# Optimization experiments

Hardware: AMD Instinct MI355X
Metric: run time of the kernel (lower is better)

Reference implementation:

```python
import math
import jax, jax.numpy as jnp
import numpy as np

CAPACITY = 2097152  # 2**21, power of two -> complete sum tree
SIZE = 1048576


def _build_tree(probs):
    # Tree layout: node i has children 2i+1, 2i+2; leaves are tree[-capacity:].
    # For power-of-two capacity this is levels concatenated root-first.
    levels = [probs]
    x = probs
    while x.shape[0] > 1:
        x = x.reshape(-1, 2).sum(axis=1)
        levels.append(x)
    return jnp.concatenate(levels[::-1])


def setup_inputs() -> dict:
    key = jax.random.key(0)
    k1, k2 = jax.random.split(key)
    priorities = jax.random.uniform(k1, (CAPACITY,), dtype=jnp.float32)
    uniform = jax.random.uniform(k2, (SIZE,), dtype=jnp.float32)
    return {"priorities": priorities, "uniform": uniform, "size": SIZE}


def reference(priorities, uniform, size):
    cap = priorities.shape[0]
    depth = int(math.log2(cap))  # number of traversal steps (complete tree)
    tree = _build_tree(priorities)  # [2*cap - 1]
    total = tree[0]

    # sample() with equal_mode=True: stratified samples in [0, total)
    offsets = jnp.linspace(0.0, total, size + 1, dtype=jnp.float32)[:-1]
    sums = uniform * total / size + offsets  # [size]
    idx0 = jnp.zeros((size,), dtype=jnp.int32)

    def body(_, carry):
        idx, s = carry
        left = 2 * idx + 1
        left_val = tree[left]            # gather [size]
        go_left = s <= left_val
        idx = jnp.where(go_left, left, left + 1)
        s = jnp.where(go_left, s, s - left_val)
        return idx, s

    idx, _ = jax.lax.fori_loop(0, depth, body, (idx0, sums))
    return idx - cap + 1  # leaf index in [0, cap)
```

## Files before the change

kernel.cpp:

```cpp
#include <hip/hip_runtime.h>


#define CAP    (1 << 21)
#define NSAMP  (1 << 20)
#define L18OFF ((1 << 18) - 1)

__global__ __launch_bounds__(256) void build_tree(const float* __restrict__ prio,
                                                  float* __restrict__ tree) {
    __shared__ __align__(16) float A[512];
    __shared__ __align__(16) float B[256];
    const int b = blockIdx.x, t = threadIdx.x;
    const float4* p4 = (const float4*)(prio + (size_t)b * 4096);

    #pragma unroll
    for (int i = t; i < 512; i += 256) {
        float4 x = p4[2 * i], y = p4[2 * i + 1];
        A[i] = ((x.x + x.y) + (x.z + x.w)) + ((y.x + y.y) + (y.z + y.w));
    }
    __syncthreads();
    {
        float* g = tree + L18OFF + b * 512;
        #pragma unroll
        for (int i = t; i < 512; i += 256) g[i] = A[i];
    }
    float* src = A;
    float* dst = B;
    int cnt = 256;
    int off = (1 << 17) - 1;
    for (int lvl = 17; lvl >= 9; --lvl) {
        for (int i = t; i < cnt; i += 256) {
            float2 v = ((const float2*)src)[i];
            float r = v.x + v.y;
            dst[i] = r;
            tree[off + b * cnt + i] = r;
        }
        __syncthreads();
        float* tmp = src; src = dst; dst = tmp;
        off = (off - 1) >> 1;
        cnt >>= 1;
    }
}

__global__ __launch_bounds__(256) void sample_kernel(const float* __restrict__ tree,
                                                     const float* __restrict__ prio,
                                                     const float* __restrict__ uniform,
                                                     int* __restrict__ out) {
    __shared__ float nds[8191];
    const int t = threadIdx.x;

    for (int i = 511 + t; i < 8191; i += 256) nds[i] = tree[i];
    __syncthreads();
    {
        int cnt = 256, off = 255;
        for (int lvl = 8; lvl >= 0; --lvl) {
            for (int i = t; i < cnt; i += 256) {
                int n = off + i;
                nds[n] = nds[2 * n + 1] + nds[2 * n + 2];
            }
            __syncthreads();
            off = (off - 1) >> 1;
            cnt >>= 1;
        }
    }

    const float total = nds[0];
    const float scale = total / (float)NSAMP;
    const int base = blockIdx.x * 1024 + t;

    float s[4];
    int   id[4];
    #pragma unroll
    for (int q = 0; q < 4; ++q) {
        int j = base + 256 * q;
        s[q]  = uniform[j] * total / (float)NSAMP + scale * (float)j;
        id[q] = 0;
    }

    #pragma unroll
    for (int d = 0; d < 12; ++d) {
        #pragma unroll
        for (int q = 0; q < 4; ++q) {
            int left = 2 * id[q] + 1;
            float lv = nds[left];
            bool r = s[q] > lv;
            s[q]  = r ? s[q] - lv : s[q];
            id[q] = r ? left + 1 : left;
        }
    }
    #pragma unroll
    for (int d = 0; d < 6; ++d) {
        #pragma unroll
        for (int q = 0; q < 4; ++q) {
            int left = 2 * id[q] + 1;
            float lv = tree[left];
            bool r = s[q] > lv;
            s[q]  = r ? s[q] - lv : s[q];
            id[q] = r ? left + 1 : left;
        }
    }
    #pragma unroll
    for (int q = 0; q < 4; ++q) {
        int p = id[q] - L18OFF;
        const float4* pp = (const float4*)prio + 2 * (size_t)p;
        float4 x = pp[0], y = pp[1];
        float l19 = (x.x + x.y) + (x.z + x.w);
        bool r1 = s[q] > l19;
        float ss = r1 ? s[q] - l19 : s[q];
        float l20 = r1 ? (y.x + y.y) : (x.x + x.y);
        bool r2 = ss > l20;
        ss = r2 ? ss - l20 : ss;
        float leaf = r1 ? (r2 ? y.z : y.x) : (r2 ? x.z : x.x);
        bool r3 = ss > leaf;
        out[base + 256 * q] = 8 * p + (r1 ? 4 : 0) + (r2 ? 2 : 0) + (r3 ? 1 : 0);
    }
}

extern "C" void kernel_launch(void* const* d_in, const int* in_sizes, int n_in,
                              void* d_out, int out_size, void* d_ws, size_t ws_size,
                              hipStream_t stream) {
    const float* prio    = (const float*)d_in[0];
    const float* uniform = (const float*)d_in[1];
    (void)in_sizes; (void)n_in; (void)out_size; (void)ws_size;

    float* tree = (float*)d_ws;

    build_tree<<<512, 256, 0, stream>>>(prio, tree);
    sample_kernel<<<NSAMP / 1024, 256, 0, stream>>>(tree, prio, uniform, (int*)d_out);
}
```

Baseline: 76.26 us.

## Fuse tree build and sampling into one kernel with a grid-wide atomic barrier

```diff
diff --git a/kernel.cpp b/kernel.cpp
--- a/kernel.cpp
+++ b/kernel.cpp
@@ -4,55 +4,54 @@
 #define CAP    (1 << 21)
 #define NSAMP  (1 << 20)
 #define L18OFF ((1 << 18) - 1)
+#define NBLK   1024
 
-__global__ __launch_bounds__(256) void build_tree(const float* __restrict__ prio,
-                                                  float* __restrict__ tree) {
-    __shared__ __align__(16) float A[512];
-    __shared__ __align__(16) float B[256];
+__global__ __launch_bounds__(256) void fused_kernel(const float* __restrict__ prio,
+                                                    const float* __restrict__ uniform,
+                                                    float* __restrict__ tree,
+                                                    unsigned int* __restrict__ bar,
+                                                    int* __restrict__ out) {
+    __shared__ __align__(16) float nds[8191];
     const int b = blockIdx.x, t = threadIdx.x;
-    const float4* p4 = (const float4*)(prio + (size_t)b * 4096);
 
-    #pragma unroll
-    for (int i = t; i < 512; i += 256) {
-        float4 x = p4[2 * i], y = p4[2 * i + 1];
-        A[i] = ((x.x + x.y) + (x.z + x.w)) + ((y.x + y.y) + (y.z + y.w));
+    {
+        const float4* p4 = (const float4*)(prio + (size_t)b * 2048);
+        float4 x = p4[2 * t], y = p4[2 * t + 1];
+        float n18 = ((x.x + x.y) + (x.z + x.w)) + ((y.x + y.y) + (y.z + y.w));
+        tree[L18OFF + b * 256 + t] = n18;
+        nds[t] = n18;
+        __syncthreads();
+        float* src = nds;
+        float* dst = nds + 4096;
+        int cnt = 128, off = (1 << 17) - 1;
+        for (int lvl = 17; lvl >= 10; --lvl) {
+            if (t < cnt) {
+                float r = src[2 * t] + src[2 * t + 1];
+                dst[t] = r;
+                tree[off + b * cnt + t] = r;
+            }
+            __syncthreads();
+            float* tmp = src; src = dst; dst = tmp;
+            off = (off - 1) >> 1;
+            cnt >>= 1;
+        }
+    }
+
+    __threadfence();
+    if (t == 0) {
+        __hip_atomic_fetch_add(bar, 1u, __ATOMIC_ACQ_REL, __HIP_MEMORY_SCOPE_AGENT);
+        while (__hip_atomic_load(bar, __ATOMIC_ACQUIRE, __HIP_MEMORY_SCOPE_AGENT) < NBLK) {
+            __builtin_amdgcn_s_sleep(8);
+        }
     }
     __syncthreads();
-    {
-        float* g = tree + L18OFF + b * 512;
-        #pragma unroll
-        for (int i = t; i < 512; i += 256) g[i] = A[i];
-    }
-    float* src = A;
-    float* dst = B;
-    int cnt = 256;
-    int off = (1 << 17) - 1;
-    for (int lvl = 17; lvl >= 9; --lvl) {
-        for (int i = t; i < cnt; i += 256) {
-            float2 v = ((const float2*)src)[i];
-            float r = v.x + v.y;
-            dst[i] = r;
-            tree[off + b * cnt + i] = r;
-        }
-        __syncthreads();
-        float* tmp = src; src = dst; dst = tmp;
-        off = (off - 1) >> 1;
-        cnt >>= 1;
-    }
-}
+    __threadfence();
 
-__global__ __launch_bounds__(256) void sample_kernel(const float* __restrict__ tree,
-                                                     const float* __restrict__ prio,
-                                                     const float* __restrict__ uniform,
-                                                     int* __restrict__ out) {
-    __shared__ float nds[8191];
-    const int t = threadIdx.x;
-
-    for (int i = 511 + t; i < 8191; i += 256) nds[i] = tree[i];
+    for (int i = 1023 + t; i < 8191; i += 256) nds[i] = tree[i];
     __syncthreads();
     {
-        int cnt = 256, off = 255;
-        for (int lvl = 8; lvl >= 0; --lvl) {
+        int cnt = 512, off = 511;
+        for (int lvl = 9; lvl >= 0; --lvl) {
             for (int i = t; i < cnt; i += 256) {
                 int n = off + i;
                 nds[n] = nds[2 * n + 1] + nds[2 * n + 2];
@@ -65,7 +64,7 @@
 
     const float total = nds[0];
     const float scale = total / (float)NSAMP;
-    const int base = blockIdx.x * 1024 + t;
+    const int base = b * 1024 + t;
 
     float s[4];
     int   id[4];
@@ -75,7 +74,6 @@
         s[q]  = uniform[j] * total / (float)NSAMP + scale * (float)j;
         id[q] = 0;
     }
-
     #pragma unroll
     for (int d = 0; d < 12; ++d) {
         #pragma unroll
@@ -123,7 +121,8 @@
     (void)in_sizes; (void)n_in; (void)out_size; (void)ws_size;
 
     float* tree = (float*)d_ws;
+    unsigned int* bar = (unsigned int*)((float*)d_ws + (1 << 20));
 
-    build_tree<<<512, 256, 0, stream>>>(prio, tree);
-    sample_kernel<<<NSAMP / 1024, 256, 0, stream>>>(tree, prio, uniform, (int*)d_out);
+    hipMemsetAsync(bar, 0, 4, stream);
+    fused_kernel<<<NBLK, 256, 0, stream>>>(prio, uniform, tree, bar, (int*)d_out);
 }
```

Measured after the change: 235.0 us. +208.1%, slower.

## Store lower tree levels as per-subtree contiguous blocks for cache-local traversal

Applied to the files above, without the earlier changes.

```diff
diff --git a/kernel.cpp b/kernel.cpp
--- a/kernel.cpp
+++ b/kernel.cpp
@@ -3,59 +3,66 @@
 
 #define CAP    (1 << 21)
 #define NSAMP  (1 << 20)
-#define L18OFF ((1 << 18) - 1)
 
 __global__ __launch_bounds__(256) void build_tree(const float* __restrict__ prio,
-                                                  float* __restrict__ tree) {
-    __shared__ __align__(16) float A[512];
-    __shared__ __align__(16) float B[256];
+                                                  float* __restrict__ tree,
+                                                  float* __restrict__ blocked) {
+    __shared__ float L18[512], L17[256], L16[128], L15[64], L14[32],
+                     L13[16],  L12[8],   L11[4],   L10[2];
+    __shared__ __align__(16) float rec[1024];
     const int b = blockIdx.x, t = threadIdx.x;
-    const float4* p4 = (const float4*)(prio + (size_t)b * 4096);
 
-    #pragma unroll
-    for (int i = t; i < 512; i += 256) {
-        float4 x = p4[2 * i], y = p4[2 * i + 1];
-        A[i] = ((x.x + x.y) + (x.z + x.w)) + ((y.x + y.y) + (y.z + y.w));
+    {
+        const float4* p4 = (const float4*)(prio + (size_t)b * 4096);
+        float4 x0 = p4[4*t+0], x1 = p4[4*t+1], x2 = p4[4*t+2], x3 = p4[4*t+3];
+        L18[2*t]   = ((x0.x+x0.y)+(x0.z+x0.w)) + ((x1.x+x1.y)+(x1.z+x1.w));
+        L18[2*t+1] = ((x2.x+x2.y)+(x2.z+x2.w)) + ((x3.x+x3.y)+(x3.z+x3.w));
     }
     __syncthreads();
-    {
-        float* g = tree + L18OFF + b * 512;
-        #pragma unroll
-        for (int i = t; i < 512; i += 256) g[i] = A[i];
+    L17[t] = L18[2*t] + L18[2*t+1];              __syncthreads();
+    if (t < 128) L16[t] = L17[2*t] + L17[2*t+1]; __syncthreads();
+    if (t <  64) L15[t] = L16[2*t] + L16[2*t+1]; __syncthreads();
+    if (t <  32) L14[t] = L15[2*t] + L15[2*t+1]; __syncthreads();
+    if (t <  16) L13[t] = L14[2*t] + L14[2*t+1]; __syncthreads();
+    if (t <   8) L12[t] = L13[2*t] + L13[2*t+1]; __syncthreads();
+    if (t <   4) L11[t] = L12[2*t] + L12[2*t+1]; __syncthreads();
+    if (t <   2) L10[t] = L11[2*t] + L11[2*t+1]; __syncthreads();
+
+    if (t < 8) tree[4095 + b*8 + t] = L12[t];
+    if (t < 4) tree[2047 + b*4 + t] = L11[t];
+    if (t < 2) tree[1023 + b*2 + t] = L10[t];
+
+    for (int i = t; i < 1024; i += 256) {
+        int r = i >> 7, off = i & 127;
+        float v = 0.0f;
+        if      (off <   2) v = L13[ 2*r + off];
+        else if (off <   6) v = L14[ 4*r + off -  2];
+        else if (off <  14) v = L15[ 8*r + off -  6];
+        else if (off <  30) v = L16[16*r + off - 14];
+        else if (off <  62) v = L17[32*r + off - 30];
+        else if (off < 126) v = L18[64*r + off - 62];
+        rec[i] = v;
     }
-    float* src = A;
-    float* dst = B;
-    int cnt = 256;
-    int off = (1 << 17) - 1;
-    for (int lvl = 17; lvl >= 9; --lvl) {
-        for (int i = t; i < cnt; i += 256) {
-            float2 v = ((const float2*)src)[i];
-            float r = v.x + v.y;
-            dst[i] = r;
-            tree[off + b * cnt + i] = r;
-        }
-        __syncthreads();
-        float* tmp = src; src = dst; dst = tmp;
-        off = (off - 1) >> 1;
-        cnt >>= 1;
-    }
+    __syncthreads();
+    ((float4*)(blocked + (size_t)b * 1024))[t] = ((const float4*)rec)[t];
 }
 
 __global__ __launch_bounds__(256) void sample_kernel(const float* __restrict__ tree,
+                                                     const float* __restrict__ blocked,
                                                      const float* __restrict__ prio,
                                                      const float* __restrict__ uniform,
                                                      int* __restrict__ out) {
     __shared__ float nds[8191];
     const int t = threadIdx.x;
 
-    for (int i = 511 + t; i < 8191; i += 256) nds[i] = tree[i];
+    for (int i = 1023 + t; i < 8191; i += 256) nds[i] = tree[i];
     __syncthreads();
     {
-        int cnt = 256, off = 255;
-        for (int lvl = 8; lvl >= 0; --lvl) {
+        int cnt = 512, off = 511;
+        for (int lvl = 9; lvl >= 0; --lvl) {
             for (int i = t; i < cnt; i += 256) {
                 int n = off + i;
-                nds[n] = nds[2 * n + 1] + nds[2 * n + 2];
+                nds[n] = nds[2*n+1] + nds[2*n+2];
             }
             __syncthreads();
             off = (off - 1) >> 1;
@@ -67,8 +74,7 @@
     const float scale = total / (float)NSAMP;
     const int base = blockIdx.x * 1024 + t;
 
-    float s[4];
-    int   id[4];
+    float s[4]; int id[4];
     #pragma unroll
     for (int q = 0; q < 4; ++q) {
         int j = base + 256 * q;
@@ -87,20 +93,31 @@
             id[q] = r ? left + 1 : left;
         }
     }
+
+    int p12[4], k[4];
     #pragma unroll
-    for (int d = 0; d < 6; ++d) {
+    for (int q = 0; q < 4; ++q) {
+        p12[q] = id[q] - 4095;
+        float lv = blocked[p12[q] << 7];
+        bool r = s[q] > lv;
+        s[q] = r ? s[q] - lv : s[q];
+        k[q] = r ? 1 : 0;
+    }
+    #pragma unroll
+    for (int d = 0; d < 5; ++d) {
         #pragma unroll
         for (int q = 0; q < 4; ++q) {
-            int left = 2 * id[q] + 1;
-            float lv = tree[left];
+            int left = 2 * k[q] + 2;
+            float lv = blocked[(p12[q] << 7) + left];
             bool r = s[q] > lv;
-            s[q]  = r ? s[q] - lv : s[q];
-            id[q] = r ? left + 1 : left;
+            s[q] = r ? s[q] - lv : s[q];
+            k[q] = r ? left + 1 : left;
         }
     }
+
     #pragma unroll
     for (int q = 0; q < 4; ++q) {
-        int p = id[q] - L18OFF;
+        int p = (p12[q] << 6) + (k[q] - 62);
         const float4* pp = (const float4*)prio + 2 * (size_t)p;
         float4 x = pp[0], y = pp[1];
         float l19 = (x.x + x.y) + (x.z + x.w);
@@ -122,8 +139,9 @@
     const float* uniform = (const float*)d_in[1];
     (void)in_sizes; (void)n_in; (void)out_size; (void)ws_size;
 
-    float* tree = (float*)d_ws;
+    float* tree    = (float*)d_ws;
+    float* blocked = (float*)d_ws + 8192;
 
-    build_tree<<<512, 256, 0, stream>>>(prio, tree);
-    sample_kernel<<<NSAMP / 1024, 256, 0, stream>>>(tree, prio, uniform, (int*)d_out);
+    build_tree<<<512, 256, 0, stream>>>(prio, tree, blocked);
+    sample_kernel<<<NSAMP / 1024, 256, 0, stream>>>(tree, blocked, prio, uniform, (int*)d_out);
 }
```

Result: no change. 76.56 us (+0.4%).
